# Kernel optimization log

Measured on AMD Instinct MI355X. Metric: run time of the kernel, lower is better.

The kernel has to match this reference:

```python
import jax, jax.numpy as jnp
import numpy as np
import math

D_MODEL = 1024
D_STATE = 16
D_CONV = 4
EXPAND = 2
D_INNER = EXPAND * D_MODEL
DT_RANK = math.ceil(D_MODEL / 16)  # 64
B_SZ, L_SEQ = 2, 2048


def setup_inputs() -> dict:
    key = jax.random.key(0)
    ks = jax.random.split(key, 10)
    s = 0.02
    x = jax.random.normal(ks[0], (B_SZ, L_SEQ, D_MODEL), dtype=jnp.float32)
    W_in = jax.random.normal(ks[1], (D_MODEL, 2 * D_INNER), dtype=jnp.float32) * s
    conv_w = jax.random.normal(ks[2], (D_INNER, 1, D_CONV), dtype=jnp.float32) * 0.3
    conv_b = jax.random.normal(ks[3], (D_INNER,), dtype=jnp.float32) * 0.01
    W_x = jax.random.normal(ks[4], (D_INNER, DT_RANK + 2 * D_STATE), dtype=jnp.float32) * s
    dt_std = DT_RANK ** (-0.5)
    W_dt = jax.random.uniform(ks[5], (DT_RANK, D_INNER), minval=-dt_std, maxval=dt_std, dtype=jnp.float32)
    # dt bias init: inverse-softplus of dt ~ logUniform[dt_min, dt_max]
    dt_min, dt_max = 1e-3, 1e-1
    dt = jnp.exp(jax.random.uniform(ks[6], (D_INNER,)) * (math.log(dt_max) - math.log(dt_min)) + math.log(dt_min))
    dt = jnp.clip(dt, 1e-4)
    b_dt = dt + jnp.log(-jnp.expm1(-dt))
    A_log = jnp.log(jnp.broadcast_to(jnp.arange(1, D_STATE + 1, dtype=jnp.float32)[None, :], (D_INNER, D_STATE)))
    D_param = jnp.ones((D_INNER,), dtype=jnp.float32)
    W_out = jax.random.normal(ks[7], (D_INNER, D_MODEL), dtype=jnp.float32) * s
    return {"x": x, "W_in": W_in, "conv_w": conv_w, "conv_b": conv_b,
            "W_x": W_x, "W_dt": W_dt, "b_dt": b_dt, "A_log": A_log,
            "D_param": D_param, "W_out": W_out}


def _silu(v):
    return v * jax.nn.sigmoid(v)


def reference(x, W_in, conv_w, conv_b, W_x, W_dt, b_dt, A_log, D_param, W_out):
    B, L, _ = x.shape
    # 1) input projection -> (x_proj, z)
    xz = x @ W_in                      # [B,L,2*Di]
    x_p, z = jnp.split(xz, 2, axis=-1)
    # 2) causal depthwise conv1d (pad left d_conv-1, truncate == causal)
    xc = jnp.transpose(x_p, (0, 2, 1))  # [B,Di,L]
    xc = jax.lax.conv_general_dilated(
        xc, conv_w, window_strides=(1,), padding=[(D_CONV - 1, 0)],
        feature_group_count=D_INNER,
        dimension_numbers=("NCH", "OIH", "NCH"))
    xc = xc + conv_b[None, :, None]
    x_conv = _silu(jnp.transpose(xc, (0, 2, 1)))  # [B,L,Di]
    # 3) input-dependent SSM params
    ssm = x_conv @ W_x                 # [B,L,dt_rank+2N]
    dtr, Bm, Cm = jnp.split(ssm, [DT_RANK, DT_RANK + D_STATE], axis=-1)
    delta = jax.nn.softplus(dtr @ W_dt + b_dt)        # [B,L,Di]
    A = -jnp.exp(A_log)                               # [Di,N]
    dA = jnp.exp(delta[..., None] * A)                # [B,L,Di,N]
    dBx = delta[..., None] * Bm[:, :, None, :] * x_conv[..., None]  # [B,L,Di,N]
    # 4) sequential scan over time via lax.scan
    def step(h, inp):
        dA_t, dBx_t, C_t = inp          # [B,Di,N],[B,Di,N],[B,N]
        h = dA_t * h + dBx_t
        y = jnp.einsum("bdn,bn->bd", h, C_t)
        return h, y
    h0 = jnp.zeros((B, D_INNER, D_STATE), dtype=x.dtype)
    _, ys = jax.lax.scan(step, h0,
                         (jnp.moveaxis(dA, 1, 0), jnp.moveaxis(dBx, 1, 0), jnp.moveaxis(Cm, 1, 0)))
    y = jnp.moveaxis(ys, 0, 1)          # [B,L,Di]
    # 5) skip, gate, output projection
    y = y + x_conv * D_param
    y = y * _silu(z)
    return y @ W_out
```

## Files before the change

### kernel.cpp

```cpp
#include <hip/hip_runtime.h>
#include <hip/hip_bf16.h>
#include <math.h>

#define B_SZ     2
#define L_SEQ    2048
#define D_MODEL  1024
#define D_STATE  16
#define D_CONV   4
#define D_INNER  2048
#define DT_RANK  64
#define NROWS    (B_SZ * L_SEQ)
#define XZ_COLS  (2 * D_INNER)
#define SSM_LD   128

#define NC 64
#define LC 32

typedef unsigned short ushort_t;
typedef __attribute__((ext_vector_type(8))) _Float16 half8;
typedef __attribute__((ext_vector_type(8))) ushort_t ushort8;
typedef __attribute__((ext_vector_type(4))) ushort_t ushort4v;
typedef __attribute__((ext_vector_type(4))) float floatx4;

static __device__ __forceinline__ ushort_t f2h(float f) {
    union { _Float16 h; ushort_t u; } c;
    c.h = (_Float16)f;
    return c.u;
}
static __device__ __forceinline__ float h2f(ushort_t u) {
    union { _Float16 h; ushort_t u; } c;
    c.u = u;
    return (float)c.h;
}

#define GLDS16(g, l)                                                        \
    __builtin_amdgcn_global_load_lds(                                       \
        (const __attribute__((address_space(1))) void*)(g),                 \
        (__attribute__((address_space(3))) void*)(l), 16, 0, 0)

static __device__ __forceinline__ void vm_wait8() {
    asm volatile("s_waitcnt vmcnt(8)" ::: "memory");
}
static __device__ __forceinline__ void vm_wait0() {
    asm volatile("s_waitcnt vmcnt(0)" ::: "memory");
}

__global__ __launch_bounds__(512, 2) void gemm1_256(const ushort_t* __restrict__ A,
                                                    const ushort_t* __restrict__ Bt,
                                                    ushort_t* __restrict__ xph,
                                                    ushort_t* __restrict__ zh) {
    __shared__ ushort_t lds[2][2][64 * 256];

    const int tid  = threadIdx.x;
    const int wave = tid >> 6;
    const int lane = tid & 63;
    int id   = blockIdx.y * 16 + blockIdx.x;
    int swz  = (id & 7) * 32 + (id >> 3);
    const int row0 = (swz >> 4) * 256;
    const int col0 = (swz & 15) * 256;

    const int wr   = (wave >> 2) * 128;
    const int wc   = (wave & 3) * 64;
    const int fr   = lane & 15;
    const int quad = lane >> 4;
    const int s_r8 = lane >> 3;
    const int s_c  = lane & 7;

    floatx4 acc[8][4];
#pragma unroll
    for (int i = 0; i < 8; i++)
#pragma unroll
        for (int j = 0; j < 4; j++) acc[i][j] = (floatx4)0.f;

    auto STAGE = [&](int t, int b) {
        int k0 = t * 64;
#pragma unroll
        for (int inst = 0; inst < 4; inst++) {
            int rb = wave * 8 + inst * 64;
            int r  = rb + s_r8;
            int lc = s_c ^ (r & 7);
            GLDS16(A  + (size_t)(row0 + r) * 1024 + k0 + lc * 8,
                   &lds[b][0][rb * 64]);
            GLDS16(Bt + (size_t)(col0 + r) * 1024 + k0 + lc * 8,
                   &lds[b][1][rb * 64]);
        }
    };

    STAGE(0, 0);
    STAGE(1, 1);
    vm_wait8();
    __builtin_amdgcn_s_barrier();

    for (int t = 0; t < 16; t++) {
        const ushort_t* As = lds[t & 1][0];
        const ushort_t* Bs = lds[t & 1][1];
#pragma unroll
        for (int ks = 0; ks < 2; ks++) {
            half8 bf[4];
#pragma unroll
            for (int j = 0; j < 4; j++) {
                int r  = wc + j * 16 + fr;
                int pc = (ks * 4 + quad) ^ (r & 7);
                bf[j] = *(const half8*)&Bs[r * 64 + pc * 8];
            }
#pragma unroll
            for (int i = 0; i < 8; i++) {
                int r  = wr + i * 16 + fr;
                int pc = (ks * 4 + quad) ^ (r & 7);
                half8 af = *(const half8*)&As[r * 64 + pc * 8];
#pragma unroll
                for (int j = 0; j < 4; j++)
                    acc[i][j] = __builtin_amdgcn_mfma_f32_16x16x32_f16(
                        af, bf[j], acc[i][j], 0, 0, 0);
            }
        }
        __builtin_amdgcn_s_barrier();
        if (t < 14) STAGE(t + 2, t & 1);
        if (t < 15) {
            if (t < 14) vm_wait8(); else vm_wait0();
            __builtin_amdgcn_s_barrier();
        }
    }

    ushort_t* cs = &lds[0][0][0];
#pragma unroll
    for (int i = 0; i < 8; i++) {
        int rl = wr + i * 16 + quad * 4;
#pragma unroll
        for (int j = 0; j < 4; j++) {
            int cl = wc + j * 16 + fr;
#pragma unroll
            for (int reg = 0; reg < 4; reg++) {
                int r  = rl + reg;
                int cp = cl ^ (((r >> 2) & 7) << 4);
                cs[(r << 8) + cp] = f2h(acc[i][j][reg]);
            }
        }
    }
    __syncthreads();
    ushort_t* dst = (col0 < 2048) ? xph : zh;
    const int cb  = col0 & 2047;
#pragma unroll
    for (int k = 0; k < 16; k++) {
        int idx = k * 512 + tid;
        int r   = idx >> 5;
        int c   = (idx & 31) * 8;
        int cp  = c ^ (((r >> 2) & 7) << 4);
        *(ushort8*)&dst[(size_t)(row0 + r) * 2048 + cb + c] =
            *(const ushort8*)&cs[(r << 8) + cp];
    }
}

__global__ __launch_bounds__(512, 2) void gemm4_dual(const ushort_t* __restrict__ A,
                                                     const ushort_t* __restrict__ Bt,
                                                     float* __restrict__ C) {
    __shared__ ushort_t ldsb[65536];

    const int tid  = threadIdx.x;
    const int wave = tid >> 6;
    const int lane = tid & 63;
    const int kw   = wave >> 2;
    const int w4   = wave & 3;
    int id   = blockIdx.y * 8 + blockIdx.x;
    int swz  = (id & 7) * 32 + (id >> 3);
    const int row0 = (swz >> 3) * 128;
    const int col0 = (swz & 7) * 128;

    const int wr   = (w4 >> 1) * 64;
    const int wc   = (w4 & 1) * 64;
    const int fr   = lane & 15;
    const int quad = lane >> 4;
    const int s_r  = lane >> 3;
    const int s_pc = lane & 7;

    floatx4 acc[4][4];
#pragma unroll
    for (int i = 0; i < 4; i++)
#pragma unroll
        for (int j = 0; j < 4; j++) acc[i][j] = (floatx4)0.f;

    auto STAGE = [&](int t, int b) {
        int k0 = kw * 1024 + t * 64;
#pragma unroll
        for (int inst = 0; inst < 4; inst++) {
            int rb = w4 * 32 + inst * 8;
            int r  = rb + s_r;
            int lc = s_pc ^ (r & 7);
            GLDS16(A  + (size_t)(row0 + r) * 2048 + k0 + lc * 8,
                   &ldsb[(kw * 2 + b) * 8192 + rb * 64]);
            GLDS16(Bt + (size_t)(col0 + r) * 2048 + k0 + lc * 8,
                   &ldsb[32768 + (kw * 2 + b) * 8192 + rb * 64]);
        }
    };

    STAGE(0, 0);
    STAGE(1, 1);
    vm_wait8();
    __builtin_amdgcn_s_barrier();

    for (int t = 0; t < 16; t++) {
        const ushort_t* as = &ldsb[(kw * 2 + (t & 1)) * 8192];
        const ushort_t* bs = &ldsb[32768 + (kw * 2 + (t & 1)) * 8192];
#pragma unroll
        for (int ks = 0; ks < 2; ks++) {
            half8 af[4], bfr[4];
#pragma unroll
            for (int i = 0; i < 4; i++) {
                int r  = wr + i * 16 + fr;
                int pc = (ks * 4 + quad) ^ (r & 7);
                af[i] = *(const half8*)&as[r * 64 + pc * 8];
            }
#pragma unroll
            for (int j = 0; j < 4; j++) {
                int r  = wc + j * 16 + fr;
                int pc = (ks * 4 + quad) ^ (r & 7);
                bfr[j] = *(const half8*)&bs[r * 64 + pc * 8];
            }
#pragma unroll
            for (int i = 0; i < 4; i++)
#pragma unroll
                for (int j = 0; j < 4; j++)
                    acc[i][j] = __builtin_amdgcn_mfma_f32_16x16x32_f16(
                        af[i], bfr[j], acc[i][j], 0, 0, 0);
        }
        __builtin_amdgcn_s_barrier();
        if (t < 14) STAGE(t + 2, t & 1);
        if (t < 15) {
            if (t < 14) vm_wait8(); else vm_wait0();
            __builtin_amdgcn_s_barrier();
        }
    }

    __syncthreads();
    float* cs = (float*)ldsb;
    if (kw == 0) {
#pragma unroll
        for (int i = 0; i < 4; i++)
#pragma unroll
            for (int j = 0; j < 4; j++) {
                int cl = wc + j * 16 + fr;
#pragma unroll
                for (int reg = 0; reg < 4; reg++) {
                    int r = wr + i * 16 + quad * 4 + reg;
                    cs[r * 132 + cl] = acc[i][j][reg];
                }
            }
    }
    __syncthreads();
    if (kw == 1) {
#pragma unroll
        for (int i = 0; i < 4; i++)
#pragma unroll
            for (int j = 0; j < 4; j++) {
                int cl = wc + j * 16 + fr;
#pragma unroll
                for (int reg = 0; reg < 4; reg++) {
                    int r = wr + i * 16 + quad * 4 + reg;
                    cs[r * 132 + cl] += acc[i][j][reg];
                }
            }
    }
    __syncthreads();
#pragma unroll
    for (int k = 0; k < 8; k++) {
        int idx = k * 512 + tid;
        int r   = idx >> 5;
        int c   = (idx & 31) * 4;
        float4 v = *(const float4*)&cs[r * 132 + c];
        *(float4*)&C[(size_t)(row0 + r) * 1024 + col0 + c] = v;
    }
}

static __device__ __forceinline__ void gemm_tile(const ushort_t* __restrict__ A,
                                                 const ushort_t* __restrict__ Bt,
                                                 int K, int row0, int col0,
                                                 int kbase, int klen,
                                                 ushort_t* As, ushort_t* Bs,
                                                 floatx4 acc[4][4]) {
    const int tid  = threadIdx.x;
    const int wave = tid >> 6;
    const int lane = tid & 63;
    const int wr   = (wave >> 1) * 64;
    const int wc   = (wave & 1) * 64;
    const int fr   = lane & 15;
    const int quad = lane >> 4;
    const int s_r  = lane >> 3;
    const int s_pc = lane & 7;

    auto STAGE = [&](int k0, int b) {
#pragma unroll
        for (int inst = 0; inst < 4; inst++) {
            int rb = wave * 32 + inst * 8;
            int r  = rb + s_r;
            int lc = s_pc ^ (r & 7);
            GLDS16(A  + (size_t)(row0 + r) * K + k0 + lc * 8, &As[b * 8192 + rb * 64]);
            GLDS16(Bt + (size_t)(col0 + r) * K + k0 + lc * 8, &Bs[b * 8192 + rb * 64]);
        }
    };

    const int nt = klen >> 6;
    STAGE(kbase, 0);
    if (nt > 1) { STAGE(kbase + 64, 1); vm_wait8(); }
    else        { vm_wait0(); }
    __builtin_amdgcn_s_barrier();

    for (int ti = 0; ti < nt; ti++) {
        const ushort_t* as = As + (ti & 1) * 8192;
        const ushort_t* bs = Bs + (ti & 1) * 8192;
#pragma unroll
        for (int ks = 0; ks < 2; ks++) {
            half8 af[4], bfr[4];
#pragma unroll
            for (int i = 0; i < 4; i++) {
                int r  = wr + i * 16 + fr;
                int pc = (ks * 4 + quad) ^ (r & 7);
                af[i] = *(const half8*)&as[r * 64 + pc * 8];
            }
#pragma unroll
            for (int j = 0; j < 4; j++) {
                int r  = wc + j * 16 + fr;
                int pc = (ks * 4 + quad) ^ (r & 7);
                bfr[j] = *(const half8*)&bs[r * 64 + pc * 8];
            }
#pragma unroll
            for (int i = 0; i < 4; i++)
#pragma unroll
                for (int j = 0; j < 4; j++)
                    acc[i][j] = __builtin_amdgcn_mfma_f32_16x16x32_f16(
                        af[i], bfr[j], acc[i][j], 0, 0, 0);
        }
        __builtin_amdgcn_s_barrier();
        if (ti + 2 < nt) STAGE(kbase + (ti + 2) * 64, ti & 1);
        if (ti + 1 < nt) {
            if (ti + 2 < nt) vm_wait8(); else vm_wait0();
            __builtin_amdgcn_s_barrier();
        }
    }
}

__global__ __launch_bounds__(256) void gemm_f16(const ushort_t* __restrict__ A,
                                                const ushort_t* __restrict__ Bt,
                                                float* __restrict__ C,
                                                ushort_t* __restrict__ C2,
                                                ushort_t* __restrict__ C3,
                                                int M, int N, int K,
                                                int kbase, int klen,
                                                int mode,
                                                const float* __restrict__ bias) {
    __shared__ ushort_t As[2 * 128 * 64];
    __shared__ ushort_t Bs[2 * 128 * 64];

    if (klen == 0) {
        klen  = K / gridDim.z;
        kbase = blockIdx.z * klen;
        C    += (size_t)blockIdx.z * M * N;
    }

    const int tid  = threadIdx.x;
    const int wave = tid >> 6;
    const int lane = tid & 63;
    const int row0 = blockIdx.y * 128;
    const int col0 = blockIdx.x * 128;
    const int wr   = (wave >> 1) * 64;
    const int wc   = (wave & 1) * 64;
    const int fr   = lane & 15;
    const int quad = lane >> 4;

    floatx4 acc[4][4];
#pragma unroll
    for (int i = 0; i < 4; i++)
#pragma unroll
        for (int j = 0; j < 4; j++) acc[i][j] = (floatx4)0.f;

    gemm_tile(A, Bt, K, row0, col0, kbase, klen, As, Bs, acc);

    if (mode == 1 || mode == 3) {
#pragma unroll
        for (int i = 0; i < 4; i++) {
            int rloc = wr + i * 16 + quad * 4;
            ushort_t* base = (rloc < 64) ? As : Bs;
#pragma unroll
            for (int j = 0; j < 4; j++) {
                int cloc = wc + j * 16 + fr;
                float bb = (mode == 1) ? bias[col0 + cloc] : 0.f;
#pragma unroll
                for (int reg = 0; reg < 4; reg++) {
                    int r = rloc + reg;
                    float v = acc[i][j][reg];
                    if (mode == 1) {
                        float xv = v + bb;
                        v = fmaxf(xv, 0.f) + __logf(1.f + __expf(-fabsf(xv)));
                    }
                    int cp = cloc ^ (((r >> 2) & 7) << 4);
                    base[((r & 63) << 7) + cp] = f2h(v);
                }
            }
        }
        __syncthreads();
#pragma unroll
        for (int k = 0; k < 8; k++) {
            int bid = k * 256 + tid;
            int r   = bid >> 4;
            int c   = (bid & 15) * 8;
            int cp  = c ^ (((r >> 2) & 7) << 4);
            const ushort_t* src = ((r < 64) ? As : Bs) + ((r & 63) << 7) + cp;
            ushort8 v = *(const ushort8*)src;
            if (mode == 1) {
                *(ushort8*)&C2[(size_t)(row0 + r) * N + col0 + c] = v;
            } else {
                if (col0 < 2048)
                    *(ushort8*)&C2[(size_t)(row0 + r) * 2048 + col0 + c] = v;
                else
                    *(ushort8*)&C3[(size_t)(row0 + r) * 2048 + (col0 - 2048) + c] = v;
            }
        }
    } else {
#pragma unroll
        for (int p = 0; p < 2; p++) {
            if (p) __syncthreads();
#pragma unroll
            for (int i = 0; i < 4; i++) {
                int rloc = wr + i * 16 + quad * 4;
                float* base = (rloc < 64) ? (float*)As : (float*)Bs;
#pragma unroll
                for (int jj = 0; jj < 2; jj++) {
                    int j  = 2 * p + jj;
                    int cl = (wc >> 1) + jj * 16 + fr;
#pragma unroll
                    for (int reg = 0; reg < 4; reg++) {
                        int r  = rloc + reg;
                        int cp = cl ^ (((r >> 2) & 7) << 2);
                        base[((r & 63) << 6) + cp] = acc[i][j][reg];
                    }
                }
            }
            __syncthreads();
#pragma unroll
            for (int k = 0; k < 8; k++) {
                int bid = k * 256 + tid;
                int r   = bid >> 4;
                int cl  = (bid & 15) * 4;
                int cp  = cl ^ (((r >> 2) & 7) << 2);
                const float* src = ((r < 64) ? (float*)As : (float*)Bs) +
                                   ((r & 63) << 6) + cp;
                float4 v = *(const float4*)src;
                int ct = (cl & 31) + (cl >> 5) * 64 + p * 32;
                *(float4*)&C[(size_t)(row0 + r) * N + col0 + ct] = v;
            }
        }
    }
}

__global__ __launch_bounds__(256) void cast_all(const float* __restrict__ x,
                                                const float* __restrict__ Win,
                                                const float* __restrict__ Wx,
                                                const float* __restrict__ Wdt,
                                                const float* __restrict__ Wout,
                                                ushort_t* __restrict__ A1,
                                                ushort_t* __restrict__ Bt1,
                                                ushort_t* __restrict__ Wxt,
                                                ushort_t* __restrict__ Wdtt,
                                                ushort_t* __restrict__ Wot) {
    __shared__ float t[32][33];
    const int bid = blockIdx.x;
    const int tid = threadIdx.x;

    if (bid < 2048) {
        int base = (bid * 256 + tid) * 8;
        const float4 a = *(const float4*)(x + base);
        const float4 b = *(const float4*)(x + base + 4);
        ushort8 o;
        o[0] = f2h(a.x); o[1] = f2h(a.y); o[2] = f2h(a.z); o[3] = f2h(a.w);
        o[4] = f2h(b.x); o[5] = f2h(b.y); o[6] = f2h(b.z); o[7] = f2h(b.w);
        *(ushort8*)(A1 + base) = o;
    } else if (bid < 6144) {
        int b2 = bid - 2048;
        int n0 = (b2 & 127) * 32;
        int k0 = (b2 >> 7) * 32;
        int c  = tid & 31;
        int r4 = tid >> 5;
#pragma unroll
        for (int p = 0; p < 4; p++) {
            int r = r4 + p * 8;
            t[r][c] = Win[(size_t)(k0 + r) * XZ_COLS + n0 + c];
        }
        __syncthreads();
#pragma unroll
        for (int p = 0; p < 4; p++) {
            int nn = r4 + p * 8;
            int kk = c;
            Bt1[(size_t)(n0 + nn) * 1024 + k0 + kk] = f2h(t[kk][nn]);
        }
    } else if (bid < 7168) {
        int idx = (bid - 6144) * 256 + tid;
        int n = idx & 127;
        int k = idx >> 7;
        float v = (n < 96) ? Wx[(size_t)k * 96 + n] : 0.f;
        Wxt[(size_t)n * 2048 + k] = f2h(v);
    } else if (bid < 7680) {
        int idx = (bid - 7168) * 256 + tid;
        int n = idx & 2047;
        int k = idx >> 11;
        ushort_t hv = f2h(Wdt[(size_t)k * 2048 + n]);
        Wdtt[(size_t)n * 128 + k]      = hv;
        Wdtt[(size_t)n * 128 + 64 + k] = hv;
    } else {
        int b4 = bid - 7680;
        int n0 = (b4 & 31) * 32;
        int k0 = (b4 >> 5) * 32;
        int c  = tid & 31;
        int r4 = tid >> 5;
#pragma unroll
        for (int p = 0; p < 4; p++) {
            int r = r4 + p * 8;
            t[r][c] = Wout[(size_t)(k0 + r) * D_MODEL + n0 + c];
        }
        __syncthreads();
#pragma unroll
        for (int p = 0; p < 4; p++) {
            int nn = r4 + p * 8;
            int kk = c;
            Wot[(size_t)(n0 + nn) * D_INNER + k0 + kk] = f2h(t[kk][nn]);
        }
    }
}

__global__ __launch_bounds__(256) void conv_silu_kernel(const ushort_t* __restrict__ xph,
                                                        const float* __restrict__ cw,
                                                        const float* __restrict__ cb,
                                                        ushort_t* __restrict__ XcS) {
    int idx = blockIdx.x * 256 + threadIdx.x;
    int d   = idx & (D_INNER - 1);
    int row = idx >> 11;
    int l   = row & (L_SEQ - 1);
    const float4 w = *(const float4*)(cw + d * 4);
    float acc = cb[d];
    if (l >= 3) acc = fmaf(h2f(xph[(size_t)(row - 3) * D_INNER + d]), w.x, acc);
    if (l >= 2) acc = fmaf(h2f(xph[(size_t)(row - 2) * D_INNER + d]), w.y, acc);
    if (l >= 1) acc = fmaf(h2f(xph[(size_t)(row - 1) * D_INNER + d]), w.z, acc);
    acc = fmaf(h2f(xph[(size_t)row * D_INNER + d]), w.w, acc);
    float s = acc / (1.f + __expf(-acc));
    XcS[idx] = f2h(s);
}

__global__ __launch_bounds__(256) void reduce_ssm_kernel(const float* __restrict__ part,
                                                         float* __restrict__ ssm,
                                                         ushort_t* __restrict__ dtrS) {
    int idx4 = (blockIdx.x * 256 + threadIdx.x) * 4;
    float4 s = make_float4(0.f, 0.f, 0.f, 0.f);
#pragma unroll
    for (int p = 0; p < 8; p++) {
        float4 v = *(const float4*)(part + (size_t)p * NROWS * SSM_LD + idx4);
        s.x += v.x; s.y += v.y; s.z += v.z; s.w += v.w;
    }
    *(float4*)(ssm + idx4) = s;
    int c = idx4 & 127;
    if (c < 64) {
        int m = idx4 >> 7;
        float sv[4] = {s.x, s.y, s.z, s.w};
        ushort4v h, l;
#pragma unroll
        for (int e = 0; e < 4; e++) {
            h[e] = f2h(sv[e]);
            l[e] = f2h(sv[e] - h2f(h[e]));
        }
        *(ushort4v*)(dtrS + (size_t)m * 128 + c)      = h;
        *(ushort4v*)(dtrS + (size_t)m * 128 + 64 + c) = l;
    }
}

static __device__ __forceinline__ void dA_powers(float r, float* dA) {
    float r2 = r * r;
    float r3 = r2 * r;
    float r4 = r2 * r2;
    float r8 = r4 * r4;
    dA[0] = r;       dA[1] = r2;      dA[2] = r3;      dA[3] = r4;
    dA[4] = r4 * r;  dA[5] = r4 * r2; dA[6] = r4 * r3; dA[7] = r8;
    dA[8]  = r8 * r;      dA[9]  = r8 * r2;     dA[10] = r8 * r3;
    dA[11] = r8 * r4;     dA[12] = r8 * r4 * r; dA[13] = r8 * r4 * r2;
    dA[14] = r8 * r4 * r3; dA[15] = r8 * r8;
}

__global__ __launch_bounds__(256) void scan_partial_kernel(
    const ushort_t* __restrict__ delta_h,
    const ushort_t* __restrict__ XcS,
    const float* __restrict__ ssm,
    const float* __restrict__ A_log,
    float* __restrict__ h_loc,
    float* __restrict__ S_sum)
{
    __shared__ float Bsh[LC * 16];
    const int tid = threadIdx.x;
    const int d   = blockIdx.x * 256 + tid;
    const int c   = blockIdx.y;
    const int b   = blockIdx.z;
    const int t0  = c * LC;

    if (tid < LC * 4) {
        int t  = tid >> 2;
        int ng = tid & 3;
        *(float4*)&Bsh[t * 16 + ng * 4] =
            *(const float4*)(ssm + (size_t)(b * L_SEQ + t0 + t) * SSM_LD + DT_RANK + ng * 4);
    }

    const float A_dn0 = -__expf(A_log[d * D_STATE]);
    const ushort_t* dptr = delta_h + (size_t)(b * L_SEQ + t0) * D_INNER + d;
    const ushort_t* xptr = XcS     + (size_t)(b * L_SEQ + t0) * D_INNER + d;

    ushort_t dvh[LC], xvh[LC];
#pragma unroll
    for (int t = 0; t < LC; t++) {
        dvh[t] = dptr[(size_t)t * D_INNER];
        xvh[t] = xptr[(size_t)t * D_INNER];
    }

    float h[16];
#pragma unroll
    for (int n = 0; n < 16; n++) h[n] = 0.f;
    float S = 0.f;

    __syncthreads();

#pragma unroll
    for (int t = 0; t < LC; t++) {
        float dv = h2f(dvh[t]);
        float xv = h2f(xvh[t]);
        S += dv;
        float dx = dv * xv;
        float dA[16];
        dA_powers(__expf(dv * A_dn0), dA);
#pragma unroll
        for (int n = 0; n < 16; n++)
            h[n] = fmaf(dA[n], h[n], dx * Bsh[t * 16 + n]);
    }

    float* hp = h_loc + (((size_t)(b * NC + c) * D_INNER + d) << 4);
#pragma unroll
    for (int n = 0; n < 16; n += 4)
        *(float4*)(hp + n) = make_float4(h[n], h[n + 1], h[n + 2], h[n + 3]);
    S_sum[(size_t)(b * NC + c) * D_INNER + d] = S;
}

__global__ __launch_bounds__(256) void scan_combine_kernel(
    float* __restrict__ h_loc,
    const float* __restrict__ S_sum,
    const float* __restrict__ A_log)
{
    int idx = blockIdx.x * 256 + threadIdx.x;
    int n = idx & 15;
    int d = (idx >> 4) & (D_INNER - 1);
    int b = idx >> 15;
    float A_dn = -__expf(A_log[d * D_STATE + n]);
    float h = 0.f;
    size_t base0 = (size_t)b * NC * D_INNER + d;
    float hl = h_loc[(base0 << 4) + n];
    float S  = S_sum[base0];
    for (int c = 0; c < NC; c++) {
        size_t base = base0 + (size_t)c * D_INNER;
        float hl_n = 0.f, S_n = 0.f;
        if (c + 1 < NC) {
            size_t bn = base + D_INNER;
            hl_n = h_loc[(bn << 4) + n];
            S_n  = S_sum[bn];
        }
        h_loc[(base << 4) + n] = h;
        h = fmaf(__expf(A_dn * S), h, hl);
        hl = hl_n; S = S_n;
    }
}

__global__ __launch_bounds__(256) void scan_final_kernel(
    const ushort_t* __restrict__ delta_h,
    const ushort_t* __restrict__ XcS,
    const float* __restrict__ ssm,
    const float* __restrict__ A_log,
    const float* __restrict__ h_init,
    const ushort_t* __restrict__ zh,
    const float* __restrict__ Dp,
    ushort_t* __restrict__ y_g)
{
    __shared__ float Bsh[LC * 16];
    __shared__ float Csh[LC * 16];
    const int tid = threadIdx.x;
    const int d   = blockIdx.x * 256 + tid;
    const int c   = blockIdx.y;
    const int b   = blockIdx.z;
    const int t0  = c * LC;

    {
        int t  = (tid & 127) >> 2;
        int ng = tid & 3;
        const float* src = ssm + (size_t)(b * L_SEQ + t0 + t) * SSM_LD + DT_RANK +
                           ((tid < 128) ? 0 : D_STATE) + ng * 4;
        if (tid < 128) *(float4*)&Bsh[t * 16 + ng * 4] = *(const float4*)src;
        else           *(float4*)&Csh[t * 16 + ng * 4] = *(const float4*)src;
    }

    const float A_dn0 = -__expf(A_log[d * D_STATE]);

    float h[16];
    const float* hp = h_init + (((size_t)(b * NC + c) * D_INNER + d) << 4);
#pragma unroll
    for (int n = 0; n < 16; n += 4)
        *(float4*)&h[n] = *(const float4*)(hp + n);

    const float Dpar = Dp[d];
    const ushort_t* dptr = delta_h + (size_t)(b * L_SEQ + t0) * D_INNER + d;
    const ushort_t* xptr = XcS     + (size_t)(b * L_SEQ + t0) * D_INNER + d;
    const ushort_t* zptr = zh      + (size_t)(b * L_SEQ + t0) * D_INNER + d;
    ushort_t*       yptr = y_g     + (size_t)(b * L_SEQ + t0) * D_INNER + d;

    ushort_t dvh[LC], xvh[LC], zvh[LC];
#pragma unroll
    for (int t = 0; t < LC; t++) {
        dvh[t] = dptr[(size_t)t * D_INNER];
        xvh[t] = xptr[(size_t)t * D_INNER];
        zvh[t] = zptr[(size_t)t * D_INNER];
    }

    __syncthreads();

#pragma unroll
    for (int t = 0; t < LC; t++) {
        float dv = h2f(dvh[t]);
        float xv = h2f(xvh[t]);
        float zv = h2f(zvh[t]);
        float dx = dv * xv;
        float dA[16];
        dA_powers(__expf(dv * A_dn0), dA);
        float yv = 0.f;
#pragma unroll
        for (int n = 0; n < 16; n++) {
            h[n] = fmaf(dA[n], h[n], dx * Bsh[t * 16 + n]);
            yv   = fmaf(h[n], Csh[t * 16 + n], yv);
        }
        float val = fmaf(xv, Dpar, yv);
        float sz  = zv / (1.f + __expf(-zv));
        yptr[(size_t)t * D_INNER] = f2h(val * sz);
    }
}

extern "C" void kernel_launch(void* const* d_in, const int* in_sizes, int n_in,
                              void* d_out, int out_size, void* d_ws, size_t ws_size,
                              hipStream_t stream) {
    const float* x      = (const float*)d_in[0];
    const float* W_in   = (const float*)d_in[1];
    const float* conv_w = (const float*)d_in[2];
    const float* conv_b = (const float*)d_in[3];
    const float* W_x    = (const float*)d_in[4];
    const float* W_dt   = (const float*)d_in[5];
    const float* b_dt   = (const float*)d_in[6];
    const float* A_log  = (const float*)d_in[7];
    const float* D_par  = (const float*)d_in[8];
    const float* W_out  = (const float*)d_in[9];
    float* out = (float*)d_out;

    float* ws = (float*)d_ws;
    float* xph_f   = ws;
    float* xcs_f   = xph_f   + (size_t)4194304;
    float* zh_f    = xcs_f   + (size_t)4194304;
    float* ssm     = zh_f    + (size_t)4194304;
    float* dtrS_f  = ssm     + (size_t)524288;
    float* deltaP  = dtrS_f  + (size_t)262144;
    float* h_loc   = deltaP  + (size_t)4194304;
    float* S_sum   = h_loc   + (size_t)4194304;
    float* yg_f    = S_sum   + (size_t)262144;
    float* wxt_f   = yg_f    + (size_t)4194304;
    float* wdtt_f  = wxt_f   + (size_t)131072;
    float* wot_f   = wdtt_f  + (size_t)131072;

    ushort_t* xph     = (ushort_t*)xph_f;
    ushort_t* A1      = (ushort_t*)xcs_f;
    ushort_t* Bt1     = (ushort_t*)(xcs_f + 2097152);
    ushort_t* XcS     = (ushort_t*)xcs_f;
    ushort_t* zh      = (ushort_t*)zh_f;
    ushort_t* dtrS    = (ushort_t*)dtrS_f;
    ushort_t* delta_h = (ushort_t*)deltaP;
    ushort_t* y_g     = (ushort_t*)yg_f;
    ushort_t* Wxt     = (ushort_t*)wxt_f;
    ushort_t* Wdtt    = (ushort_t*)wdtt_f;
    ushort_t* Wot     = (ushort_t*)wot_f;

    cast_all<<<9728, 256, 0, stream>>>(x, W_in, W_x, W_dt, W_out,
                                       A1, Bt1, Wxt, Wdtt, Wot);

    gemm1_256<<<dim3(16, 16), 512, 0, stream>>>(A1, Bt1, xph, zh);

    conv_silu_kernel<<<(NROWS * D_INNER) / 256, 256, 0, stream>>>(
        xph, conv_w, conv_b, XcS);

    gemm_f16<<<dim3(1, NROWS / 128, 8), 256, 0, stream>>>(
        XcS, Wxt, deltaP, nullptr, nullptr, NROWS, SSM_LD, 2048, 0, 0, 0, nullptr);

    reduce_ssm_kernel<<<(NROWS * SSM_LD) / 1024, 256, 0, stream>>>(deltaP, ssm, dtrS);

    gemm_f16<<<dim3(D_INNER / 128, NROWS / 128), 256, 0, stream>>>(
        dtrS, Wdtt, nullptr, delta_h, nullptr, NROWS, D_INNER, 128, 0, 128, 1, b_dt);

    scan_partial_kernel<<<dim3(8, NC, B_SZ), 256, 0, stream>>>(
        delta_h, XcS, ssm, A_log, h_loc, S_sum);
    scan_combine_kernel<<<(B_SZ * D_INNER * 16) / 256, 256, 0, stream>>>(
        h_loc, S_sum, A_log);
    scan_final_kernel<<<dim3(8, NC, B_SZ), 256, 0, stream>>>(
        delta_h, XcS, ssm, A_log, h_loc, zh, D_par, y_g);

    gemm4_dual<<<dim3(8, NROWS / 128), 512, 0, stream>>>(y_g, Wot, out);
}
```

Before: 279.8 us.

## Fuse causal depthwise conv and SiLU into the input-projection GEMM epilogue

The input-projection GEMM now computes the conv/SiLU directly in its epilogue for the x_proj half. To supply the causal halo it recomputes 16 extra preceding rows per tile with additional MFMAs. This removes the separate conv kernel and the round trip of xph through global memory. In exchange it adds redundant halo compute and changes the pipeline from a two-ahead prefetch with vmcnt waits to a simpler one-ahead stage with __syncthreads, which may expose more load latency. The scan combine loop is also restructured to prefetch four chunks ahead.

```diff
diff --git a/kernel.cpp b/kernel.cpp
--- a/kernel.cpp
+++ b/kernel.cpp
@@ -45,11 +45,13 @@
     asm volatile("s_waitcnt vmcnt(0)" ::: "memory");
 }
 
-__global__ __launch_bounds__(512, 2) void gemm1_256(const ushort_t* __restrict__ A,
-                                                    const ushort_t* __restrict__ Bt,
-                                                    ushort_t* __restrict__ xph,
-                                                    ushort_t* __restrict__ zh) {
-    __shared__ ushort_t lds[2][2][64 * 256];
+__global__ __launch_bounds__(512, 2) void gemm1_fused(const ushort_t* __restrict__ A,
+                                                      const ushort_t* __restrict__ Bt,
+                                                      ushort_t* __restrict__ XcS,
+                                                      ushort_t* __restrict__ zh,
+                                                      const float* __restrict__ cw,
+                                                      const float* __restrict__ cbias) {
+    __shared__ ushort_t lds[2 * 33792];
 
     const int tid  = threadIdx.x;
     const int wave = tid >> 6;
@@ -58,6 +60,7 @@
     int swz  = (id & 7) * 32 + (id >> 3);
     const int row0 = (swz >> 4) * 256;
     const int col0 = (swz & 15) * 256;
+    const bool is_xp = (col0 < 2048);
 
     const int wr   = (wave >> 2) * 128;
     const int wc   = (wave & 3) * 64;
@@ -71,29 +74,40 @@
     for (int i = 0; i < 8; i++)
 #pragma unroll
         for (int j = 0; j < 4; j++) acc[i][j] = (floatx4)0.f;
+    floatx4 acc_e[4];
+#pragma unroll
+    for (int j = 0; j < 4; j++) acc_e[j] = (floatx4)0.f;
 
     auto STAGE = [&](int t, int b) {
         int k0 = t * 64;
+        ushort_t* Ae = lds + b * 33792;
+        ushort_t* As = Ae + 1024;
+        ushort_t* Bs = As + 16384;
 #pragma unroll
         for (int inst = 0; inst < 4; inst++) {
             int rb = wave * 8 + inst * 64;
             int r  = rb + s_r8;
             int lc = s_c ^ (r & 7);
-            GLDS16(A  + (size_t)(row0 + r) * 1024 + k0 + lc * 8,
-                   &lds[b][0][rb * 64]);
-            GLDS16(Bt + (size_t)(col0 + r) * 1024 + k0 + lc * 8,
-                   &lds[b][1][rb * 64]);
+            GLDS16(A  + (size_t)(row0 + r) * 1024 + k0 + lc * 8, &As[rb * 64]);
+            GLDS16(Bt + (size_t)(col0 + r) * 1024 + k0 + lc * 8, &Bs[rb * 64]);
+        }
+        if (is_xp && wave < 2) {
+            int rl   = wave * 8 + s_r8;
+            int lc   = s_c ^ (rl & 7);
+            int grow = row0 - 16 + rl;
+            if (grow < 0) grow = 0;
+            GLDS16(A + (size_t)grow * 1024 + k0 + lc * 8, &Ae[wave * 8 * 64]);
         }
     };
 
     STAGE(0, 0);
-    STAGE(1, 1);
-    vm_wait8();
-    __builtin_amdgcn_s_barrier();
+    __syncthreads();
 
     for (int t = 0; t < 16; t++) {
-        const ushort_t* As = lds[t & 1][0];
-        const ushort_t* Bs = lds[t & 1][1];
+        if (t < 15) STAGE(t + 1, (t + 1) & 1);
+        const ushort_t* Ae = lds + (t & 1) * 33792;
+        const ushort_t* As = Ae + 1024;
+        const ushort_t* Bs = As + 16384;
 #pragma unroll
         for (int ks = 0; ks < 2; ks++) {
             half8 bf[4];
@@ -103,6 +117,14 @@
                 int pc = (ks * 4 + quad) ^ (r & 7);
                 bf[j] = *(const half8*)&Bs[r * 64 + pc * 8];
             }
+            if (is_xp && wave < 4) {
+                int pc = (ks * 4 + quad) ^ (fr & 7);
+                half8 ae = *(const half8*)&Ae[fr * 64 + pc * 8];
+#pragma unroll
+                for (int j = 0; j < 4; j++)
+                    acc_e[j] = __builtin_amdgcn_mfma_f32_16x16x32_f16(
+                        ae, bf[j], acc_e[j], 0, 0, 0);
+            }
 #pragma unroll
             for (int i = 0; i < 8; i++) {
                 int r  = wr + i * 16 + fr;
@@ -114,40 +136,108 @@
                         af, bf[j], acc[i][j], 0, 0, 0);
             }
         }
-        __builtin_amdgcn_s_barrier();
-        if (t < 14) STAGE(t + 2, t & 1);
-        if (t < 15) {
-            if (t < 14) vm_wait8(); else vm_wait0();
-            __builtin_amdgcn_s_barrier();
-        }
-    }
-
-    ushort_t* cs = &lds[0][0][0];
-#pragma unroll
-    for (int i = 0; i < 8; i++) {
-        int rl = wr + i * 16 + quad * 4;
-#pragma unroll
-        for (int j = 0; j < 4; j++) {
-            int cl = wc + j * 16 + fr;
-#pragma unroll
-            for (int reg = 0; reg < 4; reg++) {
-                int r  = rl + reg;
-                int cp = cl ^ (((r >> 2) & 7) << 4);
-                cs[(r << 8) + cp] = f2h(acc[i][j][reg]);
-            }
-        }
-    }
-    __syncthreads();
-    ushort_t* dst = (col0 < 2048) ? xph : zh;
-    const int cb  = col0 & 2047;
-#pragma unroll
-    for (int k = 0; k < 16; k++) {
-        int idx = k * 512 + tid;
-        int r   = idx >> 5;
-        int c   = (idx & 31) * 8;
-        int cp  = c ^ (((r >> 2) & 7) << 4);
-        *(ushort8*)&dst[(size_t)(row0 + r) * 2048 + cb + c] =
-            *(const ushort8*)&cs[(r << 8) + cp];
+        __syncthreads();
+    }
+
+    if (!is_xp) {
+        ushort_t* cs = lds;
+#pragma unroll
+        for (int i = 0; i < 8; i++) {
+            int rl = wr + i * 16 + quad * 4;
+#pragma unroll
+            for (int j = 0; j < 4; j++) {
+                int cl = wc + j * 16 + fr;
+#pragma unroll
+                for (int reg = 0; reg < 4; reg++) {
+                    int r  = rl + reg;
+                    int cp = cl ^ (((r >> 2) & 7) << 4);
+                    cs[(r << 8) + cp] = f2h(acc[i][j][reg]);
+                }
+            }
+        }
+        __syncthreads();
+        const int cb2 = col0 - 2048;
+#pragma unroll
+        for (int k = 0; k < 16; k++) {
+            int idx = k * 512 + tid;
+            int r   = idx >> 5;
+            int c   = (idx & 31) * 8;
+            int cp  = c ^ (((r >> 2) & 7) << 4);
+            *(ushort8*)&zh[(size_t)(row0 + r) * 2048 + cb2 + c] =
+                *(const ushort8*)&cs[(r << 8) + cp];
+        }
+        return;
+    }
+
+    ushort_t* E = lds;
+    const int whalf = (wave & 3) >> 1;
+    const int kq = tid & 15;
+    const int rr = tid >> 4;
+
+    for (int ch = 0; ch < 2; ch++) {
+        if (whalf == ch) {
+            const int cb0 = wc - ch * 128;
+#pragma unroll
+            for (int i = 0; i < 8; i++) {
+#pragma unroll
+                for (int j = 0; j < 4; j++) {
+                    int ccl = cb0 + j * 16 + fr;
+                    int kk = ccl >> 3, ee = ccl & 7;
+#pragma unroll
+                    for (int reg = 0; reg < 4; reg++) {
+                        int re = 16 + wr + i * 16 + quad * 4 + reg;
+                        E[re * 128 + ((kk ^ (re & 7)) << 3) + ee] =
+                            f2h(acc[i][j][reg]);
+                    }
+                }
+            }
+            if (wave < 4) {
+#pragma unroll
+                for (int j = 0; j < 4; j++) {
+                    int ccl = cb0 + j * 16 + fr;
+                    int kk = ccl >> 3, ee = ccl & 7;
+#pragma unroll
+                    for (int reg = 0; reg < 4; reg++) {
+                        int re = quad * 4 + reg;
+                        E[re * 128 + ((kk ^ (re & 7)) << 3) + ee] =
+                            f2h(acc_e[j][reg]);
+                    }
+                }
+            }
+        }
+        __syncthreads();
+
+        const int d = col0 + ch * 128 + kq * 8;
+        float4 wv[8]; float cbv[8];
+#pragma unroll
+        for (int e = 0; e < 8; e++) {
+            wv[e]  = *(const float4*)(cw + (size_t)(d + e) * 4);
+            cbv[e] = cbias[d + e];
+        }
+#pragma unroll
+        for (int pass = 0; pass < 8; pass++) {
+            int ro = pass * 32 + rr;
+            int gr = row0 + ro;
+            int l  = gr & (L_SEQ - 1);
+            int re = ro + 16;
+            half8 x0 = *(const half8*)&E[(re)     * 128 + ((kq ^ ((re)     & 7)) << 3)];
+            half8 x1 = *(const half8*)&E[(re - 1) * 128 + ((kq ^ ((re - 1) & 7)) << 3)];
+            half8 x2 = *(const half8*)&E[(re - 2) * 128 + ((kq ^ ((re - 2) & 7)) << 3)];
+            half8 x3 = *(const half8*)&E[(re - 3) * 128 + ((kq ^ ((re - 3) & 7)) << 3)];
+            ushort8 o;
+#pragma unroll
+            for (int e = 0; e < 8; e++) {
+                float a = cbv[e];
+                if (l >= 3) a = fmaf((float)x3[e], wv[e].x, a);
+                if (l >= 2) a = fmaf((float)x2[e], wv[e].y, a);
+                if (l >= 1) a = fmaf((float)x1[e], wv[e].z, a);
+                a = fmaf((float)x0[e], wv[e].w, a);
+                float s = a / (1.f + __expf(-a));
+                o[e] = f2h(s);
+            }
+            *(ushort8*)&XcS[(size_t)gr * 2048 + d] = o;
+        }
+        __syncthreads();
     }
 }
 
@@ -374,7 +464,7 @@
 
     gemm_tile(A, Bt, K, row0, col0, kbase, klen, As, Bs, acc);
 
-    if (mode == 1 || mode == 3) {
+    if (mode == 1) {
 #pragma unroll
         for (int i = 0; i < 4; i++) {
             int rloc = wr + i * 16 + quad * 4;
@@ -382,15 +472,12 @@
 #pragma unroll
             for (int j = 0; j < 4; j++) {
                 int cloc = wc + j * 16 + fr;
-                float bb = (mode == 1) ? bias[col0 + cloc] : 0.f;
+                float bb = bias[col0 + cloc];
 #pragma unroll
                 for (int reg = 0; reg < 4; reg++) {
                     int r = rloc + reg;
-                    float v = acc[i][j][reg];
-                    if (mode == 1) {
-                        float xv = v + bb;
-                        v = fmaxf(xv, 0.f) + __logf(1.f + __expf(-fabsf(xv)));
-                    }
+                    float xv = acc[i][j][reg] + bb;
+                    float v = fmaxf(xv, 0.f) + __logf(1.f + __expf(-fabsf(xv)));
                     int cp = cloc ^ (((r >> 2) & 7) << 4);
                     base[((r & 63) << 7) + cp] = f2h(v);
                 }
@@ -404,15 +491,8 @@
             int c   = (bid & 15) * 8;
             int cp  = c ^ (((r >> 2) & 7) << 4);
             const ushort_t* src = ((r < 64) ? As : Bs) + ((r & 63) << 7) + cp;
-            ushort8 v = *(const ushort8*)src;
-            if (mode == 1) {
-                *(ushort8*)&C2[(size_t)(row0 + r) * N + col0 + c] = v;
-            } else {
-                if (col0 < 2048)
-                    *(ushort8*)&C2[(size_t)(row0 + r) * 2048 + col0 + c] = v;
-                else
-                    *(ushort8*)&C3[(size_t)(row0 + r) * 2048 + (col0 - 2048) + c] = v;
-            }
+            *(ushort8*)&C2[(size_t)(row0 + r) * N + col0 + c] =
+                *(const ushort8*)src;
         }
     } else {
 #pragma unroll
@@ -525,24 +605,6 @@
     }
 }
 
-__global__ __launch_bounds__(256) void conv_silu_kernel(const ushort_t* __restrict__ xph,
-                                                        const float* __restrict__ cw,
-                                                        const float* __restrict__ cb,
-                                                        ushort_t* __restrict__ XcS) {
-    int idx = blockIdx.x * 256 + threadIdx.x;
-    int d   = idx & (D_INNER - 1);
-    int row = idx >> 11;
-    int l   = row & (L_SEQ - 1);
-    const float4 w = *(const float4*)(cw + d * 4);
-    float acc = cb[d];
-    if (l >= 3) acc = fmaf(h2f(xph[(size_t)(row - 3) * D_INNER + d]), w.x, acc);
-    if (l >= 2) acc = fmaf(h2f(xph[(size_t)(row - 2) * D_INNER + d]), w.y, acc);
-    if (l >= 1) acc = fmaf(h2f(xph[(size_t)(row - 1) * D_INNER + d]), w.z, acc);
-    acc = fmaf(h2f(xph[(size_t)row * D_INNER + d]), w.w, acc);
-    float s = acc / (1.f + __expf(-acc));
-    XcS[idx] = f2h(s);
-}
-
 __global__ __launch_bounds__(256) void reduce_ssm_kernel(const float* __restrict__ part,
                                                          float* __restrict__ ssm,
                                                          ushort_t* __restrict__ dtrS) {
@@ -653,19 +715,27 @@
     float A_dn = -__expf(A_log[d * D_STATE + n]);
     float h = 0.f;
     size_t base0 = (size_t)b * NC * D_INNER + d;
-    float hl = h_loc[(base0 << 4) + n];
-    float S  = S_sum[base0];
-    for (int c = 0; c < NC; c++) {
-        size_t base = base0 + (size_t)c * D_INNER;
-        float hl_n = 0.f, S_n = 0.f;
-        if (c + 1 < NC) {
-            size_t bn = base + D_INNER;
-            hl_n = h_loc[(bn << 4) + n];
-            S_n  = S_sum[bn];
-        }
-        h_loc[(base << 4) + n] = h;
-        h = fmaf(__expf(A_dn * S), h, hl);
-        hl = hl_n; S = S_n;
+    float hl4[4], S4[4];
+#pragma unroll
+    for (int j = 0; j < 4; j++) {
+        size_t bj = base0 + (size_t)j * D_INNER;
+        hl4[j] = h_loc[(bj << 4) + n];
+        S4[j]  = S_sum[bj];
+    }
+    for (int c0 = 0; c0 < NC; c0 += 4) {
+#pragma unroll
+        for (int j = 0; j < 4; j++) {
+            int c = c0 + j;
+            size_t base = base0 + (size_t)c * D_INNER;
+            float hl = hl4[j], S = S4[j];
+            if (c + 4 < NC) {
+                size_t bn = base + (size_t)4 * D_INNER;
+                hl4[j] = h_loc[(bn << 4) + n];
+                S4[j]  = S_sum[bn];
+            }
+            h_loc[(base << 4) + n] = h;
+            h = fmaf(__expf(A_dn * S), h, hl);
+        }
     }
 }
 
@@ -756,9 +826,9 @@
     float* out = (float*)d_out;
 
     float* ws = (float*)d_ws;
-    float* xph_f   = ws;
-    float* xcs_f   = xph_f   + (size_t)4194304;
-    float* zh_f    = xcs_f   + (size_t)4194304;
+    float* xcs_r   = ws;
+    float* ab_f    = xcs_r   + (size_t)4194304;
+    float* zh_f    = ab_f    + (size_t)4194304;
     float* ssm     = zh_f    + (size_t)4194304;
     float* dtrS_f  = ssm     + (size_t)524288;
     float* deltaP  = dtrS_f  + (size_t)262144;
@@ -769,10 +839,9 @@
     float* wdtt_f  = wxt_f   + (size_t)131072;
     float* wot_f   = wdtt_f  + (size_t)131072;
 
-    ushort_t* xph     = (ushort_t*)xph_f;
-    ushort_t* A1      = (ushort_t*)xcs_f;
-    ushort_t* Bt1     = (ushort_t*)(xcs_f + 2097152);
-    ushort_t* XcS     = (ushort_t*)xcs_f;
+    ushort_t* XcS     = (ushort_t*)xcs_r;
+    ushort_t* A1      = (ushort_t*)ab_f;
+    ushort_t* Bt1     = (ushort_t*)(ab_f + 2097152);
     ushort_t* zh      = (ushort_t*)zh_f;
     ushort_t* dtrS    = (ushort_t*)dtrS_f;
     ushort_t* delta_h = (ushort_t*)deltaP;
@@ -784,10 +853,8 @@
     cast_all<<<9728, 256, 0, stream>>>(x, W_in, W_x, W_dt, W_out,
                                        A1, Bt1, Wxt, Wdtt, Wot);
 
-    gemm1_256<<<dim3(16, 16), 512, 0, stream>>>(A1, Bt1, xph, zh);
-
-    conv_silu_kernel<<<(NROWS * D_INNER) / 256, 256, 0, stream>>>(
-        xph, conv_w, conv_b, XcS);
+    gemm1_fused<<<dim3(16, 16), 512, 0, stream>>>(A1, Bt1, XcS, zh,
+                                                  conv_w, conv_b);
 
     gemm_f16<<<dim3(1, NROWS / 128, 8), 256, 0, stream>>>(
         XcS, Wxt, deltaP, nullptr, nullptr, NROWS, SSM_LD, 2048, 0, 0, 0, nullptr);
```

Result: slower. 406.2 us (+45.1%).
